# Performance work log

Hardware: AMD Instinct MI355X
Metric: run time of the kernel (lower is better)

Reference implementation:

```python
import jax, jax.numpy as jnp
import numpy as np

S = 64        # state_size (nodes per graph == feature width)
B = 1024      # number of graphs
N = B * S     # total nodes
DEG = 16      # avg degree
E = N * DEG   # total edges
A = 16        # attractors
EPS = 1e-5


def setup_inputs() -> dict:
    key = jax.random.key(0)
    ks = jax.random.split(key, 16)
    x = jax.random.normal(ks[0], (N, 1), dtype=jnp.float32)
    # block-diagonal batched graphs: each graph has S nodes, S*DEG edges
    epg = S * DEG
    gid = jnp.arange(E, dtype=jnp.int32) // epg
    src = gid * S + jax.random.randint(ks[1], (E,), 0, S, dtype=jnp.int32)
    dst = gid * S + jax.random.randint(ks[2], (E,), 0, S, dtype=jnp.int32)
    edge_index = jnp.stack([src, dst], axis=0)
    f32 = jnp.float32
    return {
        "x": x, "edge_index": edge_index,
        # EdgeConv MLP: Linear(2,4) -> ReLU -> Linear(4,S)
        "w1": jax.random.normal(ks[3], (2, 4), f32) * 0.5,
        "b1": jnp.zeros((4,), f32),
        "w2": jax.random.normal(ks[4], (4, S), f32) * 0.3,
        "b2": jnp.zeros((S,), f32),
        # Conv1d(S,S,3,padding=1) x2
        "conv2_w": jax.random.normal(ks[5], (S, S, 3), f32) / np.sqrt(3 * S),
        "conv2_b": jnp.zeros((S,), f32),
        "conv3_w": jax.random.normal(ks[6], (S, S, 3), f32) / np.sqrt(3 * S),
        "conv3_b": jnp.zeros((S,), f32),
        # BatchNorm affine params
        "g1": jnp.ones((S,), f32), "be1": jnp.zeros((S,), f32),
        "g2": jnp.ones((S,), f32), "be2": jnp.zeros((S,), f32),
        "g3": jnp.ones((S,), f32), "be3": jnp.zeros((S,), f32),
        # MLP tail
        "wm1": jax.random.normal(ks[7], (S * S, 256), f32) / np.sqrt(S * S),
        "bm1": jnp.zeros((256,), f32),
        "wm2": jax.random.normal(ks[8], (256, 256), f32) / 16.0,
        "bm2": jnp.zeros((256,), f32),
        "wm3": jax.random.normal(ks[9], (256, 256), f32) / 16.0,
        "bm3": jnp.zeros((256,), f32),
        "wp": jax.random.normal(ks[10], (256, A), f32) / 16.0,
        "bp": jnp.zeros((A,), f32),
    }


def _bn(h, gamma, beta, axes):
    # training-mode batch norm (biased variance), per-channel
    mean = jnp.mean(h, axis=axes, keepdims=True)
    var = jnp.mean(jnp.square(h - mean), axis=axes, keepdims=True)
    inv = jax.lax.rsqrt(var + EPS)
    sh = [1] * h.ndim
    sh[1] = -1
    return (h - mean) * inv * gamma.reshape(sh) + beta.reshape(sh)


def _conv1d(h, w, b):
    # h: [B, C, L], w: [O, I, K], padding=1 -> same length
    out = jax.lax.conv_general_dilated(
        h, w, window_strides=(1,), padding=((1, 1),),
        dimension_numbers=("NCH", "OIH", "NCH"))
    return out + b[None, :, None]


def reference(x, edge_index, w1, b1, w2, b2, conv2_w, conv2_b, conv3_w, conv3_b,
              g1, be1, g2, be2, g3, be3, wm1, bm1, wm2, bm2, wm3, bm3, wp, bp):
    src, dst = edge_index[0], edge_index[1]
    # EdgeConv (aggr='add'): nn(cat[x_i, x_j - x_i]) summed at target i
    xi = x[dst]                              # [E,1] gather
    xj = x[src]                              # [E,1] gather
    m = jnp.concatenate([xi, xj - xi], axis=-1)      # [E,2]
    m = jax.nn.relu(m @ w1 + b1)                     # [E,4]
    m = m @ w2 + b2                                   # [E,S]
    out = jax.ops.segment_sum(m, dst, num_segments=N)  # [N,S] scatter-add
    # BN1 + ReLU on [N,S] (channel dim = 1)
    out = jax.nn.relu(_bn(out, g1, be1, axes=(0,)))
    # per-graph feature map: [B, S_nodes, S_feat] -> channels-first [B,S,S]
    out = out.reshape(B, S, S).swapaxes(1, 2)
    out = jax.nn.relu(_bn(_conv1d(out, conv2_w, conv2_b), g2, be2, axes=(0, 2)))
    out = jax.nn.relu(_bn(_conv1d(out, conv3_w, conv3_b), g3, be3, axes=(0, 2)))
    out = out.reshape(B, S * S)
    out = jax.nn.relu(out @ wm1 + bm1)
    out = jax.nn.relu(out @ wm2 + bm2)
    out = jax.nn.relu(out @ wm3 + bm3)
    logits = out @ wp + bp                            # [B, A]
    return jax.nn.log_softmax(logits, axis=1)
```

## Files before the change

### kernel.cpp

```cpp
#include <hip/hip_runtime.h>
#include <cstdint>
#include <cstddef>

typedef __attribute__((ext_vector_type(8))) short short8;
typedef __attribute__((ext_vector_type(8))) unsigned short ushort8;
typedef __attribute__((ext_vector_type(4))) float f32x4;

#define EPSV 1e-5f
#define NB 1024
#define NEDGE 1048576
#define EPG 1024
#define CNTF 65536.0f
#define REP 32

__device__ __forceinline__ ushort f2bf(float f) {
  uint u = __float_as_uint(f);
  return (ushort)((u + 0x7FFFu + ((u >> 16) & 1u)) >> 16);
}
__device__ __forceinline__ float bf2f(ushort u) {
  return __uint_as_float((uint)u << 16);
}

__global__ __launch_bounds__(256) void k_prepw(
    const float* __restrict__ wm1, const float* __restrict__ wm2,
    const float* __restrict__ wm3, const float* __restrict__ wp,
    const float* __restrict__ c2w, const float* __restrict__ c3w,
    ushort* __restrict__ wbf1t, ushort* __restrict__ wbf2t,
    ushort* __restrict__ wbf3t, ushort* __restrict__ wptbf,
    ushort* __restrict__ cwt2, ushort* __restrict__ cwt3,
    float* __restrict__ stats)
{
  __shared__ ushort T[64][72];
  const int tid = threadIdx.x;
  const int bb = blockIdx.x;

  if (bb < 256) {
    const int kc = bb >> 2, n0 = (bb & 3) << 6;
    const int kk = tid >> 2, np = (tid & 3) << 4;
    const float* srow = wm1 + (((size_t)(kk << 6) + kc) << 8) + n0 + np;
#pragma unroll
    for (int i = 0; i < 4; ++i) {
      const float4 v = *(const float4*)(srow + (i << 2));
      const int n = np + (i << 2);
      T[n + 0][kk] = f2bf(v.x); T[n + 1][kk] = f2bf(v.y);
      T[n + 2][kk] = f2bf(v.z); T[n + 3][kk] = f2bf(v.w);
    }
    __syncthreads();
    ushort* dst = wbf1t + ((size_t)kc << 14) + (n0 << 6);
    const int nl = tid >> 2, qk = (tid & 3) << 4;
    *(ushort8*)(dst + (nl << 6) + qk) = *(ushort8*)&T[nl][qk];
    *(ushort8*)(dst + (nl << 6) + qk + 8) = *(ushort8*)&T[nl][qk + 8];
    return;
  }
  if (bb < 320) {
    const int base = (((bb - 256) << 8) + tid) << 3;
    const int m = base >> 16;
    const int rem = base & 65535;
    const int kc = rem >> 14, within = rem & 16383;
    const int n = within >> 6, kk0 = within & 63;
    const float* src = m ? wm3 : wm2;
    ushort* dst = m ? wbf3t : wbf2t;
    ushort tmp[8];
#pragma unroll
    for (int j = 0; j < 8; ++j)
      tmp[j] = f2bf(src[(((kc << 6) | (kk0 + j)) << 8) + n]);
    *(ushort8*)&dst[rem] = *(ushort8*)&tmp[0];
    return;
  }
  if (bb == 320) {
    const int a = tid & 15, k0 = (tid >> 4) << 4;
    ushort tmp[16];
#pragma unroll
    for (int j = 0; j < 16; ++j) tmp[j] = f2bf(wp[((k0 + j) << 4) + a]);
    *(ushort8*)&wptbf[(a << 8) + k0] = *(ushort8*)&tmp[0];
    *(ushort8*)&wptbf[(a << 8) + k0 + 8] = *(ushort8*)&tmp[8];
    return;
  }
  if (bb == 417) {
    float4 z4 = make_float4(0.f, 0.f, 0.f, 0.f);
#pragma unroll
    for (int i = 0; i < 12; ++i) ((float4*)stats)[(i << 8) + tid] = z4;
    return;
  }
  const int flat = (bb - 321) * 256 + tid;
  const int m = flat >= 12288;
  const int idx = flat - (m ? 12288 : 0);
  const float* src = m ? c3w : c2w;
  ushort* dst = m ? cwt3 : cwt2;
  const int o = idx / 192, rem = idx - o * 192;
  const int kk = rem >> 6, c = rem & 63;
  dst[idx] = f2bf(src[o * 192 + c * 3 + kk]);
}

__global__ __launch_bounds__(256) void k_edge(
    const float* __restrict__ x, const int* __restrict__ ei,
    const float* __restrict__ w1, const float* __restrict__ b1,
    const float* __restrict__ w2, const float* __restrict__ b2,
    ushort* __restrict__ out0, float* __restrict__ stats1)
{
  __shared__ float xs[64];
  __shared__ float aggT[4][5][72];
  __shared__ float aggC[64][8];
  __shared__ float w1s[8], b1s[4];
  __shared__ float w2s[256], b2s[64];
  __shared__ float rs[4][64], rss[4][64];
  const int tid = threadIdx.x;
  const int b = blockIdx.x;
  const int w = tid >> 6;

  if (tid < 8) w1s[tid] = w1[tid];
  if (tid < 4) b1s[tid] = b1[tid];
  if (tid < 64) { xs[tid] = x[(b << 6) + tid]; b2s[tid] = b2[tid]; }
  w2s[tid] = w2[tid];
  for (int i = tid; i < 1440; i += 256) ((float*)aggT)[i] = 0.f;
  __syncthreads();

  const int e0 = b * EPG;
  const int4 s4 = ((const int4*)(ei + e0))[tid];
  const int4 d4 = ((const int4*)(ei + NEDGE + e0))[tid];
  float* agw = &aggT[w][0][0];
  const int sls[4] = {s4.x & 63, s4.y & 63, s4.z & 63, s4.w & 63};
  const int dls[4] = {d4.x & 63, d4.y & 63, d4.z & 63, d4.w & 63};
#pragma unroll
  for (int e = 0; e < 4; ++e) {
    const int dl = dls[e];
    const float xi = xs[dl];
    const float dx = xs[sls[e]] - xi;
#pragma unroll
    for (int j = 0; j < 4; ++j) {
      float h = fmaxf(fmaf(xi, w1s[j], fmaf(dx, w1s[4 + j], b1s[j])), 0.f);
      atomicAdd(&agw[j * 72 + dl], h);
    }
    atomicAdd(&agw[4 * 72 + dl], 1.0f);
  }
  __syncthreads();

  if (tid < 64) {
    const int n = tid;
    const float a0 = aggT[0][0][n] + aggT[1][0][n] + aggT[2][0][n] + aggT[3][0][n];
    const float a1 = aggT[0][1][n] + aggT[1][1][n] + aggT[2][1][n] + aggT[3][1][n];
    const float a2 = aggT[0][2][n] + aggT[1][2][n] + aggT[2][2][n] + aggT[3][2][n];
    const float a3v = aggT[0][3][n] + aggT[1][3][n] + aggT[2][3][n] + aggT[3][3][n];
    const float dg = aggT[0][4][n] + aggT[1][4][n] + aggT[2][4][n] + aggT[3][4][n];
    *(float4*)&aggC[n][0] = make_float4(a0, a1, a2, a3v);
    aggC[n][4] = dg;
  }
  __syncthreads();

  const int c = tid & 63, qq = tid >> 6;
  const float wc0 = w2s[c], wc1 = w2s[64 + c], wc2 = w2s[128 + c], wc3 = w2s[192 + c];
  const float b2c = b2s[c];
  float s = 0.f, ss = 0.f;
  for (int n = qq; n < 64; n += 4) {
    const float4 a = *(const float4*)&aggC[n][0];
    const float dg = aggC[n][4];
    float v = a.x * wc0 + a.y * wc1 + a.z * wc2 + a.w * wc3 + dg * b2c;
    out0[(size_t)(((b << 6) + n) << 6) + c] = f2bf(v);
    s += v; ss += v * v;
  }
  rs[qq][c] = s; rss[qq][c] = ss;
  __syncthreads();
  if (tid < 64) {
    float* dst = stats1 + ((b & (REP - 1)) << 7);
    atomicAdd(&dst[tid], rs[0][tid] + rs[1][tid] + rs[2][tid] + rs[3][tid]);
    atomicAdd(&dst[64 + tid], rss[0][tid] + rss[1][tid] + rss[2][tid] + rss[3][tid]);
  }
}

__global__ __launch_bounds__(256) void k_convm(
    const ushort* __restrict__ in,
    const float* __restrict__ stats_in,
    const float* __restrict__ gamma, const float* __restrict__ beta,
    const ushort* __restrict__ cwt, const float* __restrict__ cb,
    ushort* __restrict__ out,
    float* __restrict__ stats_out)
{
  __shared__ ushort As[64][200];
  __shared__ ushort Yt[66][72];
  __shared__ float aco[64], bco[64], cbs[64];
  __shared__ float ldsS[64], ldsSS[64];
  const int tid = threadIdx.x;
  const int b = blockIdx.x;

  if (tid < 64) {
    float sm = 0.f, sq = 0.f;
#pragma unroll 8
    for (int r = 0; r < REP; ++r) {
      sm += stats_in[(r << 7) + tid];
      sq += stats_in[(r << 7) + 64 + tid];
    }
    const float mean = sm * (1.0f / CNTF);
    const float var = sq * (1.0f / CNTF) - mean * mean;
    const float a = gamma[tid] * rsqrtf(var + EPSV);
    aco[tid] = a;
    bco[tid] = beta[tid] - mean * a;
    cbs[tid] = cb[tid];
    Yt[0][tid] = 0;
    Yt[65][tid] = 0;
  }
  __syncthreads();

  const size_t base = (size_t)b << 12;
  {
    const int lr = tid >> 2, p = (tid & 3) << 4;
    const ushort8 r0 = *(const ushort8*)&in[base + (lr << 6) + p];
    const ushort8 r1 = *(const ushort8*)&in[base + (lr << 6) + p + 8];
    ushort tmp[16];
#pragma unroll
    for (int j = 0; j < 8; ++j)
      tmp[j] = f2bf(fmaxf(fmaf(aco[p + j], bf2f(r0[j]), bco[p + j]), 0.f));
#pragma unroll
    for (int j = 0; j < 8; ++j)
      tmp[8 + j] = f2bf(fmaxf(fmaf(aco[p + 8 + j], bf2f(r1[j]), bco[p + 8 + j]), 0.f));
    *(ushort8*)&Yt[lr + 1][p] = *(ushort8*)&tmp[0];
    *(ushort8*)&Yt[lr + 1][p + 8] = *(ushort8*)&tmp[8];
  }
  {
    const ushort8* gw = (const ushort8*)cwt;
#pragma unroll
    for (int i = 0; i < 6; ++i) {
      const int e8 = (i << 8) + tid;
      const int o = e8 / 24, k8 = (e8 - o * 24) << 3;
      *(ushort8*)&As[o][k8] = gw[e8];
    }
  }
  __syncthreads();

  const int lane = tid & 63, w = tid >> 6;
  const int lm = lane & 15, q = lane >> 4;
  f32x4 acc[4];
#pragma unroll
  for (int nt = 0; nt < 4; ++nt) acc[nt] = (f32x4){0.f, 0.f, 0.f, 0.f};

#pragma unroll
  for (int kk = 0; kk < 3; ++kk) {
#pragma unroll
    for (int ks = 0; ks < 2; ++ks) {
      const short8 af = *(const short8*)&As[(w << 4) + lm][(kk << 6) + (ks << 5) + (q << 3)];
#pragma unroll
      for (int nt = 0; nt < 4; ++nt) {
        const short8 bfr = *(const short8*)&Yt[(nt << 4) + lm + kk][(ks << 5) + (q << 3)];
        acc[nt] = __builtin_amdgcn_mfma_f32_16x16x32_bf16(af, bfr, acc[nt], 0, 0, 0);
      }
    }
  }

  const int obase = (w << 4) + (q << 2);
  const float4 cb4 = *(const float4*)&cbs[obase];
  float s[4] = {0.f, 0.f, 0.f, 0.f}, ss[4] = {0.f, 0.f, 0.f, 0.f};
#pragma unroll
  for (int nt = 0; nt < 4; ++nt) {
    const int l = (nt << 4) + lm;
    float4 v = make_float4(acc[nt][0] + cb4.x, acc[nt][1] + cb4.y,
                           acc[nt][2] + cb4.z, acc[nt][3] + cb4.w);
    *(ushort4*)&out[base + (l << 6) + obase] =
        make_ushort4(f2bf(v.x), f2bf(v.y), f2bf(v.z), f2bf(v.w));
    s[0] += v.x; ss[0] += v.x * v.x;
    s[1] += v.y; ss[1] += v.y * v.y;
    s[2] += v.z; ss[2] += v.z * v.z;
    s[3] += v.w; ss[3] += v.w * v.w;
  }
#pragma unroll
  for (int i = 0; i < 4; ++i) {
#pragma unroll
    for (int off = 1; off < 16; off <<= 1) {
      s[i] += __shfl_xor(s[i], off);
      ss[i] += __shfl_xor(ss[i], off);
    }
    if (lm == 0) { ldsS[obase + i] = s[i]; ldsSS[obase + i] = ss[i]; }
  }
  __syncthreads();
  if (tid < 64) {
    float* dst = stats_out + ((b & (REP - 1)) << 7);
    atomicAdd(&dst[tid], ldsS[tid]);
    atomicAdd(&dst[64 + tid], ldsSS[tid]);
  }
}

__global__ __launch_bounds__(256) void k_mlp1(
    const ushort* __restrict__ z3, const float* __restrict__ stats3,
    const float* __restrict__ g3, const float* __restrict__ be3,
    const ushort* __restrict__ wbf1t, float* __restrict__ h1part)
{
  __shared__ ushort Ys[64][72];
  __shared__ ushort Ws[128][72];
  __shared__ float a3s[64], b3s[64];
  const int tid = threadIdx.x;
  const int bx = blockIdx.x, by = blockIdx.y, bz = blockIdx.z;

  if (tid < 64) {
    float sm = 0.f, sq = 0.f;
#pragma unroll 8
    for (int r = 0; r < REP; ++r) {
      sm += stats3[(r << 7) + tid];
      sq += stats3[(r << 7) + 64 + tid];
    }
    const float mean = sm * (1.0f / CNTF);
    const float var = sq * (1.0f / CNTF) - mean * mean;
    const float a = g3[tid] * rsqrtf(var + EPSV);
    a3s[tid] = a;
    b3s[tid] = be3[tid] - mean * a;
  }
  __syncthreads();

  const int lane = tid & 63, w = tid >> 6;
  const int lm = lane & 15, q = lane >> 4;
  const int gy = tid >> 2, py = (tid & 3) << 4;
  const int nn = tid >> 1, pp = (tid & 1) << 2;
  const int g0 = bx << 6, n0 = by << 7;

  f32x4 acc[8];
#pragma unroll
  for (int nt = 0; nt < 8; ++nt) acc[nt] = (f32x4){0.f, 0.f, 0.f, 0.f};

  const size_t ybase = ((size_t)(g0 + gy) << 12);

#pragma unroll 1
  for (int ck = 0; ck < 8; ++ck) {
    const int kc = (bz << 9) + (ck << 6);
    if (ck) __syncthreads();
    {
      const ushort* src = z3 + ybase + kc + py;
      const ushort8 r0 = *(const ushort8*)src;
      const ushort8 r1 = *(const ushort8*)(src + 8);
      ushort tmp[16];
#pragma unroll
      for (int j = 0; j < 8; ++j)
        tmp[j] = f2bf(fmaxf(fmaf(a3s[py + j], bf2f(r0[j]), b3s[py + j]), 0.f));
#pragma unroll
      for (int j = 0; j < 8; ++j)
        tmp[8 + j] = f2bf(fmaxf(fmaf(a3s[py + 8 + j], bf2f(r1[j]), b3s[py + 8 + j]), 0.f));
      *(ushort8*)&Ys[gy][py] = *(ushort8*)&tmp[0];
      *(ushort8*)&Ys[gy][py + 8] = *(ushort8*)&tmp[8];
    }
    {
      const ushort8* gw = (const ushort8*)(wbf1t + ((size_t)((bz << 3) + ck) << 14) + (n0 << 6));
#pragma unroll
      for (int i = 0; i < 4; ++i)
        *(ushort8*)&Ws[nn][(pp + i) << 3] = gw[(nn << 3) + pp + i];
    }
    __syncthreads();
#pragma unroll
    for (int ks = 0; ks < 2; ++ks) {
      const short8 af = *(const short8*)&Ys[(w << 4) + lm][(ks << 5) + (q << 3)];
#pragma unroll
      for (int nt = 0; nt < 8; ++nt) {
        const short8 bfr = *(const short8*)&Ws[(nt << 4) + lm][(ks << 5) + (q << 3)];
        acc[nt] = __builtin_amdgcn_mfma_f32_16x16x32_bf16(af, bfr, acc[nt], 0, 0, 0);
      }
    }
  }

  float* dst0 = h1part + ((size_t)bz << 18);
  const int gout = g0 + (w << 4) + (q << 2);
#pragma unroll
  for (int nt = 0; nt < 8; ++nt) {
    const int col = n0 + (nt << 4) + lm;
#pragma unroll
    for (int i = 0; i < 4; ++i)
      dst0[((size_t)(gout + i) << 8) + col] = acc[nt][i];
  }
}

__global__ __launch_bounds__(256) void k_tail(
    const float* __restrict__ h1part, const float* __restrict__ bm1,
    const ushort* __restrict__ wbf2t, const float* __restrict__ bm2,
    const ushort* __restrict__ wbf3t, const float* __restrict__ bm3,
    const ushort* __restrict__ wptbf, const float* __restrict__ bp,
    float* __restrict__ out)
{
  __shared__ ushort Ws[256][72];
  __shared__ ushort h1s[16][264];
  __shared__ ushort h2s[16][264];
  ushort* wpt = &Ws[0][0];
  const int tid = threadIdx.x;
  const int g0 = blockIdx.x << 4;
  const int lane = tid & 63, w = tid >> 6;
  const int lm = lane & 15, q = lane >> 4;
  const int gr = q << 2;

  {
    const int r = tid >> 4, c0 = (tid & 15) << 4;
    const float* srcb = h1part + ((size_t)(g0 + r) << 8) + c0;
#pragma unroll
    for (int i = 0; i < 4; ++i) {
      float4 vs = *(const float4*)(bm1 + c0 + (i << 2));
#pragma unroll
      for (int bz = 0; bz < 8; ++bz) {
        const float4 p = *(const float4*)(srcb + ((size_t)bz << 18) + (i << 2));
        vs.x += p.x; vs.y += p.y; vs.z += p.z; vs.w += p.w;
      }
      *(ushort4*)&h1s[r][c0 + (i << 2)] = make_ushort4(
          f2bf(fmaxf(vs.x, 0.f)), f2bf(fmaxf(vs.y, 0.f)),
          f2bf(fmaxf(vs.z, 0.f)), f2bf(fmaxf(vs.w, 0.f)));
    }
  }

  f32x4 acc[4];
#pragma unroll
  for (int nt = 0; nt < 4; ++nt) acc[nt] = (f32x4){0.f, 0.f, 0.f, 0.f};
#pragma unroll 1
  for (int ck = 0; ck < 4; ++ck) {
    __syncthreads();
    {
      const ushort8* gw = (const ushort8*)(wbf2t + (ck << 14));
#pragma unroll
      for (int i = 0; i < 8; ++i) {
        const int e8 = (i << 8) + tid;
        const int n = e8 >> 3, kk = (e8 & 7) << 3;
        *(ushort8*)&Ws[n][kk] = gw[e8];
      }
    }
    __syncthreads();
#pragma unroll
    for (int ks = 0; ks < 2; ++ks) {
      const short8 af = *(const short8*)&h1s[lm][(ck << 6) + (ks << 5) + (q << 3)];
#pragma unroll
      for (int nt = 0; nt < 4; ++nt) {
        const short8 bfr = *(const short8*)&Ws[(w << 6) + (nt << 4) + lm][(ks << 5) + (q << 3)];
        acc[nt] = __builtin_amdgcn_mfma_f32_16x16x32_bf16(af, bfr, acc[nt], 0, 0, 0);
      }
    }
  }
#pragma unroll
  for (int nt = 0; nt < 4; ++nt) {
    const int col = (w << 6) + (nt << 4) + lm;
    const float bv = bm2[col];
#pragma unroll
    for (int i = 0; i < 4; ++i)
      h2s[gr + i][col] = f2bf(fmaxf(acc[nt][i] + bv, 0.f));
  }

  f32x4 acc2[4];
#pragma unroll
  for (int nt = 0; nt < 4; ++nt) acc2[nt] = (f32x4){0.f, 0.f, 0.f, 0.f};
#pragma unroll 1
  for (int ck = 0; ck < 4; ++ck) {
    __syncthreads();
    {
      const ushort8* gw = (const ushort8*)(wbf3t + (ck << 14));
#pragma unroll
      for (int i = 0; i < 8; ++i) {
        const int e8 = (i << 8) + tid;
        const int n = e8 >> 3, kk = (e8 & 7) << 3;
        *(ushort8*)&Ws[n][kk] = gw[e8];
      }
    }
    __syncthreads();
#pragma unroll
    for (int ks = 0; ks < 2; ++ks) {
      const short8 af = *(const short8*)&h2s[lm][(ck << 6) + (ks << 5) + (q << 3)];
#pragma unroll
      for (int nt = 0; nt < 4; ++nt) {
        const short8 bfr = *(const short8*)&Ws[(w << 6) + (nt << 4) + lm][(ks << 5) + (q << 3)];
        acc2[nt] = __builtin_amdgcn_mfma_f32_16x16x32_bf16(af, bfr, acc2[nt], 0, 0, 0);
      }
    }
  }

  __syncthreads();
  {
    const ushort8* gw = (const ushort8*)wptbf;
#pragma unroll
    for (int i = 0; i < 2; ++i) {
      const int e8 = (i << 8) + tid;
      const int flat = e8 << 3;
      const int a = flat >> 8, kk = flat & 255;
      *(ushort8*)&wpt[a * 264 + kk] = gw[e8];
    }
  }
#pragma unroll
  for (int nt = 0; nt < 4; ++nt) {
    const int col = (w << 6) + (nt << 4) + lm;
    const float bv = bm3[col];
#pragma unroll
    for (int i = 0; i < 4; ++i)
      h2s[gr + i][col] = f2bf(fmaxf(acc2[nt][i] + bv, 0.f));
  }
  __syncthreads();

  if (w == 0) {
    f32x4 lacc = (f32x4){0.f, 0.f, 0.f, 0.f};
#pragma unroll
    for (int ks = 0; ks < 8; ++ks) {
      const short8 af = *(const short8*)&h2s[lm][(ks << 5) + (q << 3)];
      const short8 bfr = *(const short8*)&wpt[lm * 264 + (ks << 5) + (q << 3)];
      lacc = __builtin_amdgcn_mfma_f32_16x16x32_bf16(af, bfr, lacc, 0, 0, 0);
    }
    const float bpv = bp[lm];
    float lg[4], mx[4], se[4];
#pragma unroll
    for (int i = 0; i < 4; ++i) {
      lg[i] = lacc[i] + bpv;
      float m = lg[i];
#pragma unroll
      for (int off = 1; off < 16; off <<= 1) m = fmaxf(m, __shfl_xor(m, off));
      mx[i] = m;
      float e = expf(lg[i] - m);
#pragma unroll
      for (int off = 1; off < 16; off <<= 1) e += __shfl_xor(e, off);
      se[i] = e;
    }
#pragma unroll
    for (int i = 0; i < 4; ++i)
      out[((g0 + gr + i) << 4) + lm] = (lg[i] - mx[i]) - logf(se[i]);
  }
}

extern "C" void kernel_launch(void* const* d_in, const int* in_sizes, int n_in,
                              void* d_out, int out_size, void* d_ws, size_t ws_size,
                              hipStream_t stream)
{
  const float* x   = (const float*)d_in[0];
  const int*   ei  = (const int*)d_in[1];
  const float* w1  = (const float*)d_in[2];
  const float* b1  = (const float*)d_in[3];
  const float* w2  = (const float*)d_in[4];
  const float* b2  = (const float*)d_in[5];
  const float* c2w = (const float*)d_in[6];
  const float* c2b = (const float*)d_in[7];
  const float* c3w = (const float*)d_in[8];
  const float* c3b = (const float*)d_in[9];
  const float* g1  = (const float*)d_in[10];
  const float* be1 = (const float*)d_in[11];
  const float* g2  = (const float*)d_in[12];
  const float* be2 = (const float*)d_in[13];
  const float* g3  = (const float*)d_in[14];
  const float* be3 = (const float*)d_in[15];
  const float* wm1 = (const float*)d_in[16];
  const float* bm1 = (const float*)d_in[17];
  const float* wm2 = (const float*)d_in[18];
  const float* bm2 = (const float*)d_in[19];
  const float* wm3 = (const float*)d_in[20];
  const float* bm3 = (const float*)d_in[21];
  const float* wp  = (const float*)d_in[22];
  const float* bp  = (const float*)d_in[23];

  char* ws = (char*)d_ws;
  ushort* ubuf0 = (ushort*)ws;
  ushort* ubuf1 = (ushort*)(ws + ((size_t)8 << 20));
  float*  h1part = (float*)(ws + ((size_t)16 << 20));
  ushort* wbf1t = (ushort*)(ws + ((size_t)24 << 20));
  ushort* wbf2t = (ushort*)(ws + ((size_t)26 << 20));
  ushort* wbf3t = (ushort*)(ws + ((size_t)26 << 20) + (128 << 10));
  ushort* wptbf = (ushort*)(ws + ((size_t)26 << 20) + (256 << 10));
  float* stats = (float*)(ws + ((size_t)27 << 20));
  float* stats1 = stats;
  float* stats2 = stats + REP * 128;
  float* stats3 = stats + 2 * REP * 128;
  ushort* cwt2 = (ushort*)d_out;
  ushort* cwt3 = (ushort*)d_out + 12288;

  k_prepw<<<dim3(418), dim3(256), 0, stream>>>(
      wm1, wm2, wm3, wp, c2w, c3w,
      wbf1t, wbf2t, wbf3t, wptbf, cwt2, cwt3, stats);
  k_edge<<<dim3(NB), dim3(256), 0, stream>>>(x, ei, w1, b1, w2, b2, ubuf0, stats1);
  k_convm<<<dim3(NB), dim3(256), 0, stream>>>(ubuf0, stats1, g1, be1, cwt2, c2b, ubuf1, stats2);
  k_convm<<<dim3(NB), dim3(256), 0, stream>>>(ubuf1, stats2, g2, be2, cwt3, c3b, ubuf0, stats3);
  k_mlp1<<<dim3(16, 2, 8), dim3(256), 0, stream>>>(ubuf0, stats3, g3, be3, wbf1t, h1part);
  k_tail<<<dim3(64), dim3(256), 0, stream>>>(h1part, bm1, wbf2t, bm2, wbf3t, bm3,
                                             wptbf, bp, (float*)d_out);
}
```

Measured before the change: 190.8 us.

## Fuse all stages into one persistent kernel with hierarchical grid barriers

```diff
diff --git a/kernel.cpp b/kernel.cpp
--- a/kernel.cpp
+++ b/kernel.cpp
@@ -12,6 +12,9 @@
 #define EPG 1024
 #define CNTF 65536.0f
 #define REP 32
+#define MAXGRID 1024
+#define BARSLOT 64
+#define NPHASE 4
 
 __device__ __forceinline__ ushort f2bf(float f) {
   uint u = __float_as_uint(f);
@@ -21,20 +24,52 @@
   return __uint_as_float((uint)u << 16);
 }
 
-__global__ __launch_bounds__(256) void k_prepw(
+union __align__(16) SMem {
+  struct { ushort T[64][72]; } prep;
+  struct { float xs[64]; float aggT[4][5][72]; float aggC[64][8];
+           float w1s[8], b1s[4], w2s[256], b2s[64];
+           float rs[4][64], rss[4][64]; } edge;
+  struct { ushort As[64][200]; ushort Yt[66][72];
+           float aco[64], bco[64], cbs[64], ldsS[64], ldsSS[64]; } conv;
+  struct { ushort Ys[32][72]; ushort Ws[64][72];
+           float a3s[64], b3s[64]; } mlp;
+  struct { ushort h1s[16][264]; ushort h2s[16][264]; } tail;
+};
+
+__device__ __forceinline__ void gbar(unsigned* bar, int phase, int bid,
+                                     int nblk, int tid)
+{
+  __syncthreads();
+  if (tid == 0) {
+    const int lf = bid & 31;
+    unsigned* leaf = bar + (size_t)(phase * 33 + lf) * BARSLOT;
+    unsigned* root = bar + (size_t)(phase * 33 + 32) * BARSLOT;
+    const unsigned leafcnt = (unsigned)((nblk + 31 - lf) >> 5);
+    const unsigned nleaf = (unsigned)(nblk < 32 ? nblk : 32);
+    __threadfence();
+    unsigned old = __hip_atomic_fetch_add(leaf, 1u, __ATOMIC_ACQ_REL,
+                                          __HIP_MEMORY_SCOPE_AGENT);
+    if (old >= leafcnt - 1)
+      __hip_atomic_fetch_add(root, 1u, __ATOMIC_ACQ_REL,
+                             __HIP_MEMORY_SCOPE_AGENT);
+    while (__hip_atomic_load(root, __ATOMIC_ACQUIRE,
+                             __HIP_MEMORY_SCOPE_AGENT) < nleaf)
+      __builtin_amdgcn_s_sleep(8);
+  }
+  __syncthreads();
+}
+
+__device__ __forceinline__ void prep_body(
+    SMem& sm, const int bb, const int tid,
     const float* __restrict__ wm1, const float* __restrict__ wm2,
     const float* __restrict__ wm3, const float* __restrict__ wp,
     const float* __restrict__ c2w, const float* __restrict__ c3w,
     ushort* __restrict__ wbf1t, ushort* __restrict__ wbf2t,
     ushort* __restrict__ wbf3t, ushort* __restrict__ wptbf,
-    ushort* __restrict__ cwt2, ushort* __restrict__ cwt3,
-    float* __restrict__ stats)
-{
-  __shared__ ushort T[64][72];
-  const int tid = threadIdx.x;
-  const int bb = blockIdx.x;
-
+    ushort* __restrict__ cwt2, ushort* __restrict__ cwt3)
+{
   if (bb < 256) {
+    auto& T = sm.prep.T;
     const int kc = bb >> 2, n0 = (bb & 3) << 6;
     const int kk = tid >> 2, np = (tid & 3) << 4;
     const float* srow = wm1 + (((size_t)(kk << 6) + kc) << 8) + n0 + np;
@@ -76,59 +111,47 @@
     *(ushort8*)&wptbf[(a << 8) + k0 + 8] = *(ushort8*)&tmp[8];
     return;
   }
-  if (bb == 417) {
-    float4 z4 = make_float4(0.f, 0.f, 0.f, 0.f);
-#pragma unroll
-    for (int i = 0; i < 12; ++i) ((float4*)stats)[(i << 8) + tid] = z4;
-    return;
-  }
   const int flat = (bb - 321) * 256 + tid;
   const int m = flat >= 12288;
   const int idx = flat - (m ? 12288 : 0);
   const float* src = m ? c3w : c2w;
   ushort* dst = m ? cwt3 : cwt2;
   const int o = idx / 192, rem = idx - o * 192;
-  const int kk = rem >> 6, c = rem & 63;
-  dst[idx] = f2bf(src[o * 192 + c * 3 + kk]);
-}
-
-__global__ __launch_bounds__(256) void k_edge(
+  const int kk = rem >> 6, cc = rem & 63;
+  dst[idx] = f2bf(src[o * 192 + cc * 3 + kk]);
+}
+
+__device__ __forceinline__ void edge_body(
+    SMem& sm, const int b, const int tid,
     const float* __restrict__ x, const int* __restrict__ ei,
     const float* __restrict__ w1, const float* __restrict__ b1,
     const float* __restrict__ w2, const float* __restrict__ b2,
     ushort* __restrict__ out0, float* __restrict__ stats1)
 {
-  __shared__ float xs[64];
-  __shared__ float aggT[4][5][72];
-  __shared__ float aggC[64][8];
-  __shared__ float w1s[8], b1s[4];
-  __shared__ float w2s[256], b2s[64];
-  __shared__ float rs[4][64], rss[4][64];
-  const int tid = threadIdx.x;
-  const int b = blockIdx.x;
+  auto& E = sm.edge;
   const int w = tid >> 6;
-
-  if (tid < 8) w1s[tid] = w1[tid];
-  if (tid < 4) b1s[tid] = b1[tid];
-  if (tid < 64) { xs[tid] = x[(b << 6) + tid]; b2s[tid] = b2[tid]; }
-  w2s[tid] = w2[tid];
-  for (int i = tid; i < 1440; i += 256) ((float*)aggT)[i] = 0.f;
+  __syncthreads();
+  if (tid < 8) E.w1s[tid] = w1[tid];
+  if (tid < 4) E.b1s[tid] = b1[tid];
+  if (tid < 64) { E.xs[tid] = x[(b << 6) + tid]; E.b2s[tid] = b2[tid]; }
+  E.w2s[tid] = w2[tid];
+  for (int i = tid; i < 1440; i += 256) (&E.aggT[0][0][0])[i] = 0.f;
   __syncthreads();
 
   const int e0 = b * EPG;
   const int4 s4 = ((const int4*)(ei + e0))[tid];
   const int4 d4 = ((const int4*)(ei + NEDGE + e0))[tid];
-  float* agw = &aggT[w][0][0];
+  float* agw = &E.aggT[w][0][0];
   const int sls[4] = {s4.x & 63, s4.y & 63, s4.z & 63, s4.w & 63};
   const int dls[4] = {d4.x & 63, d4.y & 63, d4.z & 63, d4.w & 63};
 #pragma unroll
   for (int e = 0; e < 4; ++e) {
     const int dl = dls[e];
-    const float xi = xs[dl];
-    const float dx = xs[sls[e]] - xi;
+    const float xi = E.xs[dl];
+    const float dx = E.xs[sls[e]] - xi;
 #pragma unroll
     for (int j = 0; j < 4; ++j) {
-      float h = fmaxf(fmaf(xi, w1s[j], fmaf(dx, w1s[4 + j], b1s[j])), 0.f);
+      float h = fmaxf(fmaf(xi, E.w1s[j], fmaf(dx, E.w1s[4 + j], E.b1s[j])), 0.f);
       atomicAdd(&agw[j * 72 + dl], h);
     }
     atomicAdd(&agw[4 * 72 + dl], 1.0f);
@@ -137,66 +160,60 @@
 
   if (tid < 64) {
     const int n = tid;
-    const float a0 = aggT[0][0][n] + aggT[1][0][n] + aggT[2][0][n] + aggT[3][0][n];
-    const float a1 = aggT[0][1][n] + aggT[1][1][n] + aggT[2][1][n] + aggT[3][1][n];
-    const float a2 = aggT[0][2][n] + aggT[1][2][n] + aggT[2][2][n] + aggT[3][2][n];
-    const float a3v = aggT[0][3][n] + aggT[1][3][n] + aggT[2][3][n] + aggT[3][3][n];
-    const float dg = aggT[0][4][n] + aggT[1][4][n] + aggT[2][4][n] + aggT[3][4][n];
-    *(float4*)&aggC[n][0] = make_float4(a0, a1, a2, a3v);
-    aggC[n][4] = dg;
+    const float a0 = E.aggT[0][0][n] + E.aggT[1][0][n] + E.aggT[2][0][n] + E.aggT[3][0][n];
+    const float a1 = E.aggT[0][1][n] + E.aggT[1][1][n] + E.aggT[2][1][n] + E.aggT[3][1][n];
+    const float a2 = E.aggT[0][2][n] + E.aggT[1][2][n] + E.aggT[2][2][n] + E.aggT[3][2][n];
+    const float a3v = E.aggT[0][3][n] + E.aggT[1][3][n] + E.aggT[2][3][n] + E.aggT[3][3][n];
+    const float dg = E.aggT[0][4][n] + E.aggT[1][4][n] + E.aggT[2][4][n] + E.aggT[3][4][n];
+    *(float4*)&E.aggC[n][0] = make_float4(a0, a1, a2, a3v);
+    E.aggC[n][4] = dg;
   }
   __syncthreads();
 
   const int c = tid & 63, qq = tid >> 6;
-  const float wc0 = w2s[c], wc1 = w2s[64 + c], wc2 = w2s[128 + c], wc3 = w2s[192 + c];
-  const float b2c = b2s[c];
+  const float wc0 = E.w2s[c], wc1 = E.w2s[64 + c], wc2 = E.w2s[128 + c], wc3 = E.w2s[192 + c];
+  const float b2c = E.b2s[c];
   float s = 0.f, ss = 0.f;
   for (int n = qq; n < 64; n += 4) {
-    const float4 a = *(const float4*)&aggC[n][0];
-    const float dg = aggC[n][4];
+    const float4 a = *(const float4*)&E.aggC[n][0];
+    const float dg = E.aggC[n][4];
     float v = a.x * wc0 + a.y * wc1 + a.z * wc2 + a.w * wc3 + dg * b2c;
     out0[(size_t)(((b << 6) + n) << 6) + c] = f2bf(v);
     s += v; ss += v * v;
   }
-  rs[qq][c] = s; rss[qq][c] = ss;
+  E.rs[qq][c] = s; E.rss[qq][c] = ss;
   __syncthreads();
   if (tid < 64) {
     float* dst = stats1 + ((b & (REP - 1)) << 7);
-    atomicAdd(&dst[tid], rs[0][tid] + rs[1][tid] + rs[2][tid] + rs[3][tid]);
-    atomicAdd(&dst[64 + tid], rss[0][tid] + rss[1][tid] + rss[2][tid] + rss[3][tid]);
-  }
-}
-
-__global__ __launch_bounds__(256) void k_convm(
-    const ushort* __restrict__ in,
-    const float* __restrict__ stats_in,
+    atomicAdd(&dst[tid], E.rs[0][tid] + E.rs[1][tid] + E.rs[2][tid] + E.rs[3][tid]);
+    atomicAdd(&dst[64 + tid], E.rss[0][tid] + E.rss[1][tid] + E.rss[2][tid] + E.rss[3][tid]);
+  }
+}
+
+__device__ __forceinline__ void conv_body(
+    SMem& sm, const int b, const int tid,
+    const ushort* __restrict__ in, const float* __restrict__ stats_in,
     const float* __restrict__ gamma, const float* __restrict__ beta,
     const ushort* __restrict__ cwt, const float* __restrict__ cb,
-    ushort* __restrict__ out,
-    float* __restrict__ stats_out)
-{
-  __shared__ ushort As[64][200];
-  __shared__ ushort Yt[66][72];
-  __shared__ float aco[64], bco[64], cbs[64];
-  __shared__ float ldsS[64], ldsSS[64];
-  const int tid = threadIdx.x;
-  const int b = blockIdx.x;
-
+    ushort* __restrict__ out, float* __restrict__ stats_out)
+{
+  auto& C = sm.conv;
+  __syncthreads();
   if (tid < 64) {
-    float sm = 0.f, sq = 0.f;
+    float smv = 0.f, sq = 0.f;
 #pragma unroll 8
     for (int r = 0; r < REP; ++r) {
-      sm += stats_in[(r << 7) + tid];
+      smv += stats_in[(r << 7) + tid];
       sq += stats_in[(r << 7) + 64 + tid];
     }
-    const float mean = sm * (1.0f / CNTF);
+    const float mean = smv * (1.0f / CNTF);
     const float var = sq * (1.0f / CNTF) - mean * mean;
     const float a = gamma[tid] * rsqrtf(var + EPSV);
-    aco[tid] = a;
-    bco[tid] = beta[tid] - mean * a;
-    cbs[tid] = cb[tid];
-    Yt[0][tid] = 0;
-    Yt[65][tid] = 0;
+    C.aco[tid] = a;
+    C.bco[tid] = beta[tid] - mean * a;
+    C.cbs[tid] = cb[tid];
+    C.Yt[0][tid] = 0;
+    C.Yt[65][tid] = 0;
   }
   __syncthreads();
 
@@ -208,12 +225,12 @@
     ushort tmp[16];
 #pragma unroll
     for (int j = 0; j < 8; ++j)
-      tmp[j] = f2bf(fmaxf(fmaf(aco[p + j], bf2f(r0[j]), bco[p + j]), 0.f));
+      tmp[j] = f2bf(fmaxf(fmaf(C.aco[p + j], bf2f(r0[j]), C.bco[p + j]), 0.f));
 #pragma unroll
     for (int j = 0; j < 8; ++j)
-      tmp[8 + j] = f2bf(fmaxf(fmaf(aco[p + 8 + j], bf2f(r1[j]), bco[p + 8 + j]), 0.f));
-    *(ushort8*)&Yt[lr + 1][p] = *(ushort8*)&tmp[0];
-    *(ushort8*)&Yt[lr + 1][p + 8] = *(ushort8*)&tmp[8];
+      tmp[8 + j] = f2bf(fmaxf(fmaf(C.aco[p + 8 + j], bf2f(r1[j]), C.bco[p + 8 + j]), 0.f));
+    *(ushort8*)&C.Yt[lr + 1][p] = *(ushort8*)&tmp[0];
+    *(ushort8*)&C.Yt[lr + 1][p + 8] = *(ushort8*)&tmp[8];
   }
   {
     const ushort8* gw = (const ushort8*)cwt;
@@ -221,7 +238,7 @@
     for (int i = 0; i < 6; ++i) {
       const int e8 = (i << 8) + tid;
       const int o = e8 / 24, k8 = (e8 - o * 24) << 3;
-      *(ushort8*)&As[o][k8] = gw[e8];
+      *(ushort8*)&C.As[o][k8] = gw[e8];
     }
   }
   __syncthreads();
@@ -236,17 +253,17 @@
   for (int kk = 0; kk < 3; ++kk) {
 #pragma unroll
     for (int ks = 0; ks < 2; ++ks) {
-      const short8 af = *(const short8*)&As[(w << 4) + lm][(kk << 6) + (ks << 5) + (q << 3)];
+      const short8 af = *(const short8*)&C.As[(w << 4) + lm][(kk << 6) + (ks << 5) + (q << 3)];
 #pragma unroll
       for (int nt = 0; nt < 4; ++nt) {
-        const short8 bfr = *(const short8*)&Yt[(nt << 4) + lm + kk][(ks << 5) + (q << 3)];
+        const short8 bfr = *(const short8*)&C.Yt[(nt << 4) + lm + kk][(ks << 5) + (q << 3)];
         acc[nt] = __builtin_amdgcn_mfma_f32_16x16x32_bf16(af, bfr, acc[nt], 0, 0, 0);
       }
     }
   }
 
   const int obase = (w << 4) + (q << 2);
-  const float4 cb4 = *(const float4*)&cbs[obase];
+  const float4 cb4 = *(const float4*)&C.cbs[obase];
   float s[4] = {0.f, 0.f, 0.f, 0.f}, ss[4] = {0.f, 0.f, 0.f, 0.f};
 #pragma unroll
   for (int nt = 0; nt < 4; ++nt) {
@@ -267,51 +284,52 @@
       s[i] += __shfl_xor(s[i], off);
       ss[i] += __shfl_xor(ss[i], off);
     }
-    if (lm == 0) { ldsS[obase + i] = s[i]; ldsSS[obase + i] = ss[i]; }
+    if (lm == 0) { C.ldsS[obase + i] = s[i]; C.ldsSS[obase + i] = ss[i]; }
   }
   __syncthreads();
   if (tid < 64) {
     float* dst = stats_out + ((b & (REP - 1)) << 7);
-    atomicAdd(&dst[tid], ldsS[tid]);
-    atomicAdd(&dst[64 + tid], ldsSS[tid]);
-  }
-}
-
-__global__ __launch_bounds__(256) void k_mlp1(
+    atomicAdd(&dst[tid], C.ldsS[tid]);
+    atomicAdd(&dst[64 + tid], C.ldsSS[tid]);
+  }
+}
+
+__device__ __forceinline__ void mlp_body(
+    SMem& sm, const int bid, const int tid,
     const ushort* __restrict__ z3, const float* __restrict__ stats3,
     const float* __restrict__ g3, const float* __restrict__ be3,
     const ushort* __restrict__ wbf1t, float* __restrict__ h1part)
 {
-  __shared__ ushort Ys[64][72];
-  __shared__ ushort Ws[128][72];
-  __shared__ float a3s[64], b3s[64];
-  const int tid = threadIdx.x;
-  const int bx = blockIdx.x, by = blockIdx.y, bz = blockIdx.z;
-
+  auto& M = sm.mlp;
+  const int bz = bid >> 7;
+  const int bx = (bid >> 2) & 31;
+  const int by = bid & 3;
+  __syncthreads();
   if (tid < 64) {
-    float sm = 0.f, sq = 0.f;
+    float sme = 0.f, sq = 0.f;
 #pragma unroll 8
     for (int r = 0; r < REP; ++r) {
-      sm += stats3[(r << 7) + tid];
+      sme += stats3[(r << 7) + tid];
       sq += stats3[(r << 7) + 64 + tid];
     }
-    const float mean = sm * (1.0f / CNTF);
+    const float mean = sme * (1.0f / CNTF);
     const float var = sq * (1.0f / CNTF) - mean * mean;
     const float a = g3[tid] * rsqrtf(var + EPSV);
-    a3s[tid] = a;
-    b3s[tid] = be3[tid] - mean * a;
+    M.a3s[tid] = a;
+    M.b3s[tid] = be3[tid] - mean * a;
   }
   __syncthreads();
 
   const int lane = tid & 63, w = tid >> 6;
   const int lm = lane & 15, q = lane >> 4;
-  const int gy = tid >> 2, py = (tid & 3) << 4;
-  const int nn = tid >> 1, pp = (tid & 1) << 2;
-  const int g0 = bx << 6, n0 = by << 7;
-
-  f32x4 acc[8];
-#pragma unroll
-  for (int nt = 0; nt < 8; ++nt) acc[nt] = (f32x4){0.f, 0.f, 0.f, 0.f};
+  const int wr = w >> 1, wc = w & 1;
+  const int gy = tid >> 3, py = (tid & 7) << 3;
+  const int nn = tid >> 2, pw = tid & 3;
+  const int g0 = bx << 5, n0 = by << 6;
+
+  f32x4 acc[2];
+#pragma unroll
+  for (int nt = 0; nt < 2; ++nt) acc[nt] = (f32x4){0.f, 0.f, 0.f, 0.f};
 
   const size_t ybase = ((size_t)(g0 + gy) << 12);
 
@@ -320,65 +338,56 @@
     const int kc = (bz << 9) + (ck << 6);
     if (ck) __syncthreads();
     {
-      const ushort* src = z3 + ybase + kc + py;
-      const ushort8 r0 = *(const ushort8*)src;
-      const ushort8 r1 = *(const ushort8*)(src + 8);
-      ushort tmp[16];
+      const ushort8 r0 = *(const ushort8*)(z3 + ybase + kc + py);
+      ushort tmp[8];
 #pragma unroll
       for (int j = 0; j < 8; ++j)
-        tmp[j] = f2bf(fmaxf(fmaf(a3s[py + j], bf2f(r0[j]), b3s[py + j]), 0.f));
-#pragma unroll
-      for (int j = 0; j < 8; ++j)
-        tmp[8 + j] = f2bf(fmaxf(fmaf(a3s[py + 8 + j], bf2f(r1[j]), b3s[py + 8 + j]), 0.f));
-      *(ushort8*)&Ys[gy][py] = *(ushort8*)&tmp[0];
-      *(ushort8*)&Ys[gy][py + 8] = *(ushort8*)&tmp[8];
+        tmp[j] = f2bf(fmaxf(fmaf(M.a3s[py + j], bf2f(r0[j]), M.b3s[py + j]), 0.f));
+      *(ushort8*)&M.Ys[gy][py] = *(ushort8*)&tmp[0];
     }
     {
-      const ushort8* gw = (const ushort8*)(wbf1t + ((size_t)((bz << 3) + ck) << 14) + (n0 << 6));
-#pragma unroll
-      for (int i = 0; i < 4; ++i)
-        *(ushort8*)&Ws[nn][(pp + i) << 3] = gw[(nn << 3) + pp + i];
+      const ushort8* gw = (const ushort8*)(wbf1t + ((size_t)((bz << 3) + ck) << 14) + ((size_t)n0 << 6));
+      *(ushort8*)&M.Ws[nn][pw << 4] = gw[(nn << 3) + (pw << 1)];
+      *(ushort8*)&M.Ws[nn][(pw << 4) + 8] = gw[(nn << 3) + (pw << 1) + 1];
     }
     __syncthreads();
 #pragma unroll
     for (int ks = 0; ks < 2; ++ks) {
-      const short8 af = *(const short8*)&Ys[(w << 4) + lm][(ks << 5) + (q << 3)];
-#pragma unroll
-      for (int nt = 0; nt < 8; ++nt) {
-        const short8 bfr = *(const short8*)&Ws[(nt << 4) + lm][(ks << 5) + (q << 3)];
+      const short8 af = *(const short8*)&M.Ys[(wr << 4) + lm][(ks << 5) + (q << 3)];
+#pragma unroll
+      for (int nt = 0; nt < 2; ++nt) {
+        const short8 bfr = *(const short8*)&M.Ws[(wc << 5) + (nt << 4) + lm][(ks << 5) + (q << 3)];
         acc[nt] = __builtin_amdgcn_mfma_f32_16x16x32_bf16(af, bfr, acc[nt], 0, 0, 0);
       }
     }
   }
 
   float* dst0 = h1part + ((size_t)bz << 18);
-  const int gout = g0 + (w << 4) + (q << 2);
-#pragma unroll
-  for (int nt = 0; nt < 8; ++nt) {
-    const int col = n0 + (nt << 4) + lm;
+  const int gout = g0 + (wr << 4) + (q << 2);
+#pragma unroll
+  for (int nt = 0; nt < 2; ++nt) {
+    const int col = n0 + (wc << 5) + (nt << 4) + lm;
 #pragma unroll
     for (int i = 0; i < 4; ++i)
       dst0[((size_t)(gout + i) << 8) + col] = acc[nt][i];
   }
 }
 
-__global__ __launch_bounds__(256) void k_tail(
+__device__ __forceinline__ void tail_body(
+    SMem& sm, const int bid, const int tid,
     const float* __restrict__ h1part, const float* __restrict__ bm1,
     const ushort* __restrict__ wbf2t, const float* __restrict__ bm2,
     const ushort* __restrict__ wbf3t, const float* __restrict__ bm3,
     const ushort* __restrict__ wptbf, const float* __restrict__ bp,
     float* __restrict__ out)
 {
-  __shared__ ushort Ws[256][72];
-  __shared__ ushort h1s[16][264];
-  __shared__ ushort h2s[16][264];
-  ushort* wpt = &Ws[0][0];
-  const int tid = threadIdx.x;
-  const int g0 = blockIdx.x << 4;
+  auto& T = sm.tail;
+  const int g0 = bid << 4;
   const int lane = tid & 63, w = tid >> 6;
   const int lm = lane & 15, q = lane >> 4;
   const int gr = q << 2;
 
+  __syncthreads();
   {
     const int r = tid >> 4, c0 = (tid & 15) << 4;
     const float* srcb = h1part + ((size_t)(g0 + r) << 8) + c0;
@@ -390,34 +399,25 @@
         const float4 p = *(const float4*)(srcb + ((size_t)bz << 18) + (i << 2));
         vs.x += p.x; vs.y += p.y; vs.z += p.z; vs.w += p.w;
       }
-      *(ushort4*)&h1s[r][c0 + (i << 2)] = make_ushort4(
+      *(ushort4*)&T.h1s[r][c0 + (i << 2)] = make_ushort4(
           f2bf(fmaxf(vs.x, 0.f)), f2bf(fmaxf(vs.y, 0.f)),
           f2bf(fmaxf(vs.z, 0.f)), f2bf(fmaxf(vs.w, 0.f)));
     }
   }
+  __syncthreads();
 
   f32x4 acc[4];
 #pragma unroll
   for (int nt = 0; nt < 4; ++nt) acc[nt] = (f32x4){0.f, 0.f, 0.f, 0.f};
-#pragma unroll 1
+#pragma unroll
   for (int ck = 0; ck < 4; ++ck) {
-    __syncthreads();
-    {
-      const ushort8* gw = (const ushort8*)(wbf2t + (ck << 14));
-#pragma unroll
-      for (int i = 0; i < 8; ++i) {
-        const int e8 = (i << 8) + tid;
-        const int n = e8 >> 3, kk = (e8 & 7) << 3;
-        *(ushort8*)&Ws[n][kk] = gw[e8];
-      }
-    }
-    __syncthreads();
 #pragma unroll
     for (int ks = 0; ks < 2; ++ks) {
-      const short8 af = *(const short8*)&h1s[lm][(ck << 6) + (ks << 5) + (q << 3)];
+      const short8 af = *(const short8*)&T.h1s[lm][(ck << 6) + (ks << 5) + (q << 3)];
 #pragma unroll
       for (int nt = 0; nt < 4; ++nt) {
-        const short8 bfr = *(const short8*)&Ws[(w << 6) + (nt << 4) + lm][(ks << 5) + (q << 3)];
+        const int n = (w << 6) + (nt << 4) + lm;
+        const short8 bfr = *(const short8*)&wbf2t[((size_t)ck << 14) + (n << 6) + (ks << 5) + (q << 3)];
         acc[nt] = __builtin_amdgcn_mfma_f32_16x16x32_bf16(af, bfr, acc[nt], 0, 0, 0);
       }
     }
@@ -428,54 +428,34 @@
     const float bv = bm2[col];
 #pragma unroll
     for (int i = 0; i < 4; ++i)
-      h2s[gr + i][col] = f2bf(fmaxf(acc[nt][i] + bv, 0.f));
-  }
+      T.h2s[gr + i][col] = f2bf(fmaxf(acc[nt][i] + bv, 0.f));
+  }
+  __syncthreads();
 
   f32x4 acc2[4];
 #pragma unroll
   for (int nt = 0; nt < 4; ++nt) acc2[nt] = (f32x4){0.f, 0.f, 0.f, 0.f};
-#pragma unroll 1
+#pragma unroll
   for (int ck = 0; ck < 4; ++ck) {
-    __syncthreads();
-    {
-      const ushort8* gw = (const ushort8*)(wbf3t + (ck << 14));
-#pragma unroll
-      for (int i = 0; i < 8; ++i) {
-        const int e8 = (i << 8) + tid;
-        const int n = e8 >> 3, kk = (e8 & 7) << 3;
-        *(ushort8*)&Ws[n][kk] = gw[e8];
-      }
-    }
-    __syncthreads();
 #pragma unroll
     for (int ks = 0; ks < 2; ++ks) {
-      const short8 af = *(const short8*)&h2s[lm][(ck << 6) + (ks << 5) + (q << 3)];
+      const short8 af = *(const short8*)&T.h2s[lm][(ck << 6) + (ks << 5) + (q << 3)];
 #pragma unroll
       for (int nt = 0; nt < 4; ++nt) {
-        const short8 bfr = *(const short8*)&Ws[(w << 6) + (nt << 4) + lm][(ks << 5) + (q << 3)];
+        const int n = (w << 6) + (nt << 4) + lm;
+        const short8 bfr = *(const short8*)&wbf3t[((size_t)ck << 14) + (n << 6) + (ks << 5) + (q << 3)];
         acc2[nt] = __builtin_amdgcn_mfma_f32_16x16x32_bf16(af, bfr, acc2[nt], 0, 0, 0);
       }
     }
   }
-
-  __syncthreads();
-  {
-    const ushort8* gw = (const ushort8*)wptbf;
-#pragma unroll
-    for (int i = 0; i < 2; ++i) {
-      const int e8 = (i << 8) + tid;
-      const int flat = e8 << 3;
-      const int a = flat >> 8, kk = flat & 255;
-      *(ushort8*)&wpt[a * 264 + kk] = gw[e8];
-    }
-  }
+  __syncthreads();
 #pragma unroll
   for (int nt = 0; nt < 4; ++nt) {
     const int col = (w << 6) + (nt << 4) + lm;
     const float bv = bm3[col];
 #pragma unroll
     for (int i = 0; i < 4; ++i)
-      h2s[gr + i][col] = f2bf(fmaxf(acc2[nt][i] + bv, 0.f));
+      T.h2s[gr + i][col] = f2bf(fmaxf(acc2[nt][i] + bv, 0.f));
   }
   __syncthreads();
 
@@ -483,8 +463,8 @@
     f32x4 lacc = (f32x4){0.f, 0.f, 0.f, 0.f};
 #pragma unroll
     for (int ks = 0; ks < 8; ++ks) {
-      const short8 af = *(const short8*)&h2s[lm][(ks << 5) + (q << 3)];
-      const short8 bfr = *(const short8*)&wpt[lm * 264 + (ks << 5) + (q << 3)];
+      const short8 af = *(const short8*)&T.h2s[lm][(ks << 5) + (q << 3)];
+      const short8 bfr = *(const short8*)&wptbf[(lm << 8) + (ks << 5) + (q << 3)];
       lacc = __builtin_amdgcn_mfma_f32_16x16x32_bf16(af, bfr, lacc, 0, 0, 0);
     }
     const float bpv = bp[lm];
@@ -505,6 +485,119 @@
     for (int i = 0; i < 4; ++i)
       out[((g0 + gr + i) << 4) + lm] = (lg[i] - mx[i]) - logf(se[i]);
   }
+}
+
+__global__ __launch_bounds__(256, 4) void k_all(
+    const float* __restrict__ x, const int* __restrict__ ei,
+    const float* __restrict__ w1, const float* __restrict__ b1,
+    const float* __restrict__ w2, const float* __restrict__ b2,
+    const float* __restrict__ c2w, const float* __restrict__ c2b,
+    const float* __restrict__ c3w, const float* __restrict__ c3b,
+    const float* __restrict__ g1, const float* __restrict__ be1,
+    const float* __restrict__ g2, const float* __restrict__ be2,
+    const float* __restrict__ g3, const float* __restrict__ be3,
+    const float* __restrict__ wm1, const float* __restrict__ bm1,
+    const float* __restrict__ wm2, const float* __restrict__ bm2,
+    const float* __restrict__ wm3, const float* __restrict__ bm3,
+    const float* __restrict__ wp, const float* __restrict__ bp,
+    ushort* __restrict__ ubuf0, ushort* __restrict__ ubuf1,
+    float* __restrict__ h1part,
+    ushort* __restrict__ wbf1t, ushort* __restrict__ wbf2t,
+    ushort* __restrict__ wbf3t, ushort* __restrict__ wptbf,
+    ushort* __restrict__ cwt2, ushort* __restrict__ cwt3,
+    float* __restrict__ stats, unsigned* __restrict__ bar,
+    float* __restrict__ out, int nblk)
+{
+  __shared__ SMem sm;
+  const int tid = threadIdx.x;
+  const int bid = blockIdx.x;
+  float* stats1 = stats;
+  float* stats2 = stats + REP * 128;
+  float* stats3 = stats + 2 * REP * 128;
+
+  for (int it = bid; it < 417 + NB; it += nblk) {
+    if (it < 417)
+      prep_body(sm, it, tid, wm1, wm2, wm3, wp, c2w, c3w,
+                wbf1t, wbf2t, wbf3t, wptbf, cwt2, cwt3);
+    else
+      edge_body(sm, it - 417, tid, x, ei, w1, b1, w2, b2, ubuf0, stats1);
+  }
+  gbar(bar, 0, bid, nblk, tid);
+  for (int it = bid; it < NB; it += nblk)
+    conv_body(sm, it, tid, ubuf0, stats1, g1, be1, cwt2, c2b, ubuf1, stats2);
+  gbar(bar, 1, bid, nblk, tid);
+  for (int it = bid; it < NB; it += nblk)
+    conv_body(sm, it, tid, ubuf1, stats2, g2, be2, cwt3, c3b, ubuf0, stats3);
+  gbar(bar, 2, bid, nblk, tid);
+  for (int it = bid; it < NB; it += nblk)
+    mlp_body(sm, it, tid, ubuf0, stats3, g3, be3, wbf1t, h1part);
+  gbar(bar, 3, bid, nblk, tid);
+  for (int it = bid; it < 64; it += nblk)
+    tail_body(sm, it, tid, h1part, bm1, wbf2t, bm2, wbf3t, bm3, wptbf, bp, out);
+}
+
+__global__ __launch_bounds__(256) void k_prepw(
+    const float* __restrict__ wm1, const float* __restrict__ wm2,
+    const float* __restrict__ wm3, const float* __restrict__ wp,
+    const float* __restrict__ c2w, const float* __restrict__ c3w,
+    ushort* __restrict__ wbf1t, ushort* __restrict__ wbf2t,
+    ushort* __restrict__ wbf3t, ushort* __restrict__ wptbf,
+    ushort* __restrict__ cwt2, ushort* __restrict__ cwt3,
+    float* __restrict__ stats)
+{
+  __shared__ SMem sm;
+  const int tid = threadIdx.x;
+  const int bb = blockIdx.x;
+  if (bb == 417) {
+    float4 z4 = make_float4(0.f, 0.f, 0.f, 0.f);
+#pragma unroll
+    for (int i = 0; i < 12; ++i) ((float4*)stats)[(i << 8) + tid] = z4;
+    return;
+  }
+  prep_body(sm, bb, tid, wm1, wm2, wm3, wp, c2w, c3w,
+            wbf1t, wbf2t, wbf3t, wptbf, cwt2, cwt3);
+}
+
+__global__ __launch_bounds__(256) void k_edge(
+    const float* __restrict__ x, const int* __restrict__ ei,
+    const float* __restrict__ w1, const float* __restrict__ b1,
+    const float* __restrict__ w2, const float* __restrict__ b2,
+    ushort* __restrict__ out0, float* __restrict__ stats1)
+{
+  __shared__ SMem sm;
+  edge_body(sm, blockIdx.x, threadIdx.x, x, ei, w1, b1, w2, b2, out0, stats1);
+}
+
+__global__ __launch_bounds__(256) void k_convm(
+    const ushort* __restrict__ in, const float* __restrict__ stats_in,
+    const float* __restrict__ gamma, const float* __restrict__ beta,
+    const ushort* __restrict__ cwt, const float* __restrict__ cb,
+    ushort* __restrict__ out, float* __restrict__ stats_out)
+{
+  __shared__ SMem sm;
+  conv_body(sm, blockIdx.x, threadIdx.x, in, stats_in, gamma, beta, cwt, cb,
+            out, stats_out);
+}
+
+__global__ __launch_bounds__(256) void k_mlp1f(
+    const ushort* __restrict__ z3, const float* __restrict__ stats3,
+    const float* __restrict__ g3, const float* __restrict__ be3,
+    const ushort* __restrict__ wbf1t, float* __restrict__ h1part)
+{
+  __shared__ SMem sm;
+  mlp_body(sm, blockIdx.x, threadIdx.x, z3, stats3, g3, be3, wbf1t, h1part);
+}
+
+__global__ __launch_bounds__(256) void k_tailf(
+    const float* __restrict__ h1part, const float* __restrict__ bm1,
+    const ushort* __restrict__ wbf2t, const float* __restrict__ bm2,
+    const ushort* __restrict__ wbf3t, const float* __restrict__ bm3,
+    const ushort* __restrict__ wptbf, const float* __restrict__ bp,
+    float* __restrict__ out)
+{
+  __shared__ SMem sm;
+  tail_body(sm, blockIdx.x, threadIdx.x, h1part, bm1, wbf2t, bm2, wbf3t, bm3,
+            wptbf, bp, out);
 }
 
 extern "C" void kernel_launch(void* const* d_in, const int* in_sizes, int n_in,
@@ -548,16 +641,42 @@
   float* stats1 = stats;
   float* stats2 = stats + REP * 128;
   float* stats3 = stats + 2 * REP * 128;
+  unsigned* bar = (unsigned*)(ws + ((size_t)27 << 20) + 49152);
   ushort* cwt2 = (ushort*)d_out;
   ushort* cwt3 = (ushort*)d_out + 12288;
-
-  k_prepw<<<dim3(418), dim3(256), 0, stream>>>(
-      wm1, wm2, wm3, wp, c2w, c3w,
-      wbf1t, wbf2t, wbf3t, wptbf, cwt2, cwt3, stats);
-  k_edge<<<dim3(NB), dim3(256), 0, stream>>>(x, ei, w1, b1, w2, b2, ubuf0, stats1);
-  k_convm<<<dim3(NB), dim3(256), 0, stream>>>(ubuf0, stats1, g1, be1, cwt2, c2b, ubuf1, stats2);
-  k_convm<<<dim3(NB), dim3(256), 0, stream>>>(ubuf1, stats2, g2, be2, cwt3, c3b, ubuf0, stats3);
-  k_mlp1<<<dim3(16, 2, 8), dim3(256), 0, stream>>>(ubuf0, stats3, g3, be3, wbf1t, h1part);
-  k_tail<<<dim3(64), dim3(256), 0, stream>>>(h1part, bm1, wbf2t, bm2, wbf3t, bm3,
-                                             wptbf, bp, (float*)d_out);
-}
+  float* outp = (float*)d_out;
+
+  static int nblk_cached = -1;
+  if (nblk_cached < 0) {
+    int ncu = 0, maxb = 0;
+    hipError_t e1 = hipDeviceGetAttribute(&ncu, hipDeviceAttributeMultiprocessorCount, 0);
+    hipError_t e2 = hipOccupancyMaxActiveBlocksPerMultiprocessor(&maxb, k_all, 256, 0);
+    if (e1 == hipSuccess && e2 == hipSuccess && ncu > 0 && maxb > 0) {
+      long t = (long)ncu * (long)maxb;
+      nblk_cached = (int)(t < MAXGRID ? t : MAXGRID);
+    } else {
+      nblk_cached = 0;
+    }
+  }
+  const int nblk = nblk_cached;
+
+  if (nblk > 0) {
+    hipMemsetAsync(stats, 0, 49152 + NPHASE * 33 * BARSLOT * 4, stream);
+    k_all<<<dim3(nblk), dim3(256), 0, stream>>>(
+        x, ei, w1, b1, w2, b2, c2w, c2b, c3w, c3b,
+        g1, be1, g2, be2, g3, be3,
+        wm1, bm1, wm2, bm2, wm3, bm3, wp, bp,
+        ubuf0, ubuf1, h1part, wbf1t, wbf2t, wbf3t, wptbf,
+        cwt2, cwt3, stats, bar, outp, nblk);
+  } else {
+    k_prepw<<<dim3(418), dim3(256), 0, stream>>>(
+        wm1, wm2, wm3, wp, c2w, c3w,
+        wbf1t, wbf2t, wbf3t, wptbf, cwt2, cwt3, stats);
+    k_edge<<<dim3(NB), dim3(256), 0, stream>>>(x, ei, w1, b1, w2, b2, ubuf0, stats1);
+    k_convm<<<dim3(NB), dim3(256), 0, stream>>>(ubuf0, stats1, g1, be1, cwt2, c2b, ubuf1, stats2);
+    k_convm<<<dim3(NB), dim3(256), 0, stream>>>(ubuf1, stats2, g2, be2, cwt3, c3b, ubuf0, stats3);
+    k_mlp1f<<<dim3(NB), dim3(256), 0, stream>>>(ubuf0, stats3, g3, be3, wbf1t, h1part);
+    k_tailf<<<dim3(64), dim3(256), 0, stream>>>(h1part, bm1, wbf2t, bm2, wbf3t, bm3,
+                                                wptbf, bp, outp);
+  }
+}
```

Measured after the change: 338.7 us. 1.77x slower.
